# Optimization experiments

Measured on AMD Instinct MI355X. Metric: run time of the kernel, lower is better.

## Reference

```python
import jax, jax.numpy as jnp
import numpy as np

# static config (matches init_kwargs)
T_K = 3      # Time_kernel
K = 3        # spatial_kernel_side_length
C = 64       # dim_hidden
H = 4        # num_head
D = 16       # dim_head
NL = 2       # num_layers
F = 3        # dim_feature
N, S1, S2 = 32, 32, 32
P = K // 2
L1 = T_K // 2
M = T_K * K * K
EPS = 1e-5


def _neighbor_mask():
    # spatial_neighbor_mask with an all-ones city mask: offset (k1,k2) is a valid
    # neighbor of cell (s1,s2) iff it lands inside the grid.
    m = np.zeros((S1, S2, K, K), dtype=bool)
    s1 = np.arange(S1); s2 = np.arange(S2)
    for k1 in range(K):
        v1 = (s1 + k1 - P >= 0) & (s1 + k1 - P < S1)
        for k2 in range(K):
            v2 = (s2 + k2 - P >= 0) & (s2 + k2 - P < S2)
            m[:, :, k1, k2] = v1[:, None] & v2[None, :]
    mf = m.reshape(S1, S2, K * K)
    # tiled across Time_kernel, flattened in (t, k1, k2) order like the torch code
    return np.tile(mf[:, :, None, :], (1, 1, T_K, 1)).reshape(S1, S2, M)

_MASK = jnp.asarray(_neighbor_mask())


def _forward(x, W_in, b_in, W_out, b_out, Wq, bq, Wk, bk, Wv, bv):
    # BatchNorm2d (training-mode batch stats, affine = identity init)
    mean = x.mean(axis=(0, 1, 2))
    var = ((x - mean) ** 2).mean(axis=(0, 1, 2))
    h = (x - mean) * jax.lax.rsqrt(var + EPS)
    h = h @ W_in + b_in  # [N,S1,S2,C]

    for l in range(NL):
        res = h  # res_block_thickness = 1 -> residual every layer
        q = (h @ Wq[l] + bq[l]).reshape(N, S1, S2, H, D)
        # spatial unfold (nn.Unfold, padding=K//2, stride=1)
        hp = jnp.pad(h, ((0, 0), (P, P), (P, P), (0, 0)))
        u = jnp.stack([jnp.stack([hp[:, k1:k1 + S1, k2:k2 + S2, :]
                                  for k2 in range(K)]) for k1 in range(K)])  # [K,K,N,S1,S2,C]
        # time unfold (zero-padded shifts along N)
        up = jnp.pad(u, ((0, 0), (0, 0), (L1, L1), (0, 0), (0, 0), (0, 0)))
        ut = jnp.stack([up[:, :, t:t + N] for t in range(T_K)])  # [T,K,K,N,S1,S2,C]
        # per-offset single-Linear MLPs (kernel_neurons=[C,C]), batched over T,K,K
        ks = jnp.einsum('tijnabc,tijcd->nabtijd', ut, Wk[l]) + bk[l]
        vs = jnp.einsum('tijnabc,tijcd->nabtijd', ut, Wv[l]) + bv[l]
        kM = ks.reshape(N, S1, S2, M, H, D)
        vM = vs.reshape(N, S1, S2, M, H, D)
        # unscaled dot-product attention over valid neighbors (masked == dropped)
        sc = jnp.einsum('nabmhd,nabhd->nabhm', kM, q)
        sc = jnp.where(_MASK[None, :, :, None, :], sc, -1e30)
        w = jax.nn.softmax(sc, axis=-1)
        h = jnp.einsum('nabhm,nabmhd->nabhd', w, vM).reshape(N, S1, S2, C)
        h = h + res

    return h @ W_out + b_out  # [N,S1,S2,F]


def setup_inputs() -> dict:
    key = jax.random.key(0)
    k = jax.random.split(key, 11)
    s = 0.05
    return {
        'x': jax.random.normal(k[0], (N, S1, S2, F), jnp.float32),
        'W_in': jax.random.normal(k[1], (F, C), jnp.float32) * s,
        'b_in': jax.random.normal(k[2], (C,), jnp.float32) * s,
        'W_out': jax.random.normal(k[3], (C, F), jnp.float32) * s,
        'b_out': jax.random.normal(k[4], (F,), jnp.float32) * s,
        'Wq': jax.random.normal(k[5], (NL, C, C), jnp.float32) * s,
        'bq': jax.random.normal(k[6], (NL, C), jnp.float32) * s,
        'Wk': jax.random.normal(k[7], (NL, T_K, K, K, C, C), jnp.float32) * s,
        'bk': jax.random.normal(k[8], (NL, T_K, K, K, C), jnp.float32) * s,
        'Wv': jax.random.normal(k[9], (NL, T_K, K, K, C, C), jnp.float32) * s,
        'bv': jax.random.normal(k[10], (NL, T_K, K, K, C), jnp.float32) * s,
    }


def reference(x, W_in, b_in, W_out, b_out, Wq, bq, Wk, bk, Wv, bv):
    return _forward(x, W_in, b_in, W_out, b_out, Wq, bq, Wk, bk, Wv, bv)
```

## Files before the change

### kernel.cpp

```cpp
#include <hip/hip_runtime.h>
#include <hip/hip_bf16.h>


typedef short short8_t __attribute__((ext_vector_type(8)));
typedef float floatx16 __attribute__((ext_vector_type(16)));

__device__ __forceinline__ short f2bs(float f) {
    __hip_bfloat16 h = __float2bfloat16(f);
    return *reinterpret_cast<short*>(&h);
}
__device__ __forceinline__ float bs2f(short s) {
    union { unsigned u; float f; } v;
    v.u = ((unsigned)(unsigned short)s) << 16;
    return v.f;
}
__device__ __forceinline__ int hn_idx(int rowid, int chunk) {
    return rowid * 64 + ((chunk ^ (rowid & 7)) << 3);
}
__device__ __forceinline__ float half_sum(float p) {
    float a = p, b = p;
    asm("v_permlane32_swap_b32 %0, %1" : "+v"(a), "+v"(b));
    return a + b;
}

__global__ void prep_kernel(const float* __restrict__ Wq, const float* __restrict__ Wk,
                            const float* __restrict__ Wv, const float* __restrict__ bq,
                            const float* __restrict__ bk, const float* __restrict__ bv,
                            short* __restrict__ dst,
                            const float* __restrict__ x, float* __restrict__ sums) {
    if (blockIdx.x < 110) {
        __shared__ float Wf[4096];
        __shared__ float Bf[64];
        const int mat = blockIdx.x;
        const float *W, *B;
        if (mat < 2)       { W = Wq + mat * 4096;        B = bq + mat * 64; }
        else if (mat < 56) { W = Wk + (mat - 2) * 4096;  B = bk + (mat - 2) * 64; }
        else               { W = Wv + (mat - 56) * 4096; B = bv + (mat - 56) * 64; }
        const float4* W4 = (const float4*)W;
        #pragma unroll
        for (int i = 0; i < 4; ++i) {
            const int idx = threadIdx.x + i * 256;
            *(float4*)&Wf[idx * 4] = W4[idx];
        }
        if (threadIdx.x < 64) Bf[threadIdx.x] = B[threadIdx.x];
        __syncthreads();
        #pragma unroll
        for (int u = 0; u < 3; ++u) {
            const int t2 = u * 256 + threadIdx.x;
            if (t2 >= 640) break;
            const int hp = t2 / 320, rem = t2 - hp * 320;
            const int kk = rem >> 6, lane = rem & 63;
            short8_t v = {0, 0, 0, 0, 0, 0, 0, 0};
            if (kk < 4) {
                const int krow = kk * 16 + ((lane >> 5) << 3);
                const int col  = hp * 32 + (lane & 31);
                #pragma unroll
                for (int j = 0; j < 8; ++j) v[j] = f2bs(Wf[(krow + j) * 64 + col]);
            } else if ((lane >> 5) == 0) {
                const float b = Bf[hp * 32 + (lane & 31)];
                const short hi = f2bs(b);
                v[0] = hi;
                v[1] = f2bs(b - bs2f(hi));
            }
            *(short8_t*)&dst[(size_t)mat * 5120 + t2 * 8] = v;
        }
    } else {
        int bid = blockIdx.x - 110;
        int t = bid * 256 + threadIdx.x;
        const float4* x4 = (const float4*)x;
        float4 v0 = x4[t * 3 + 0], v1 = x4[t * 3 + 1], v2 = x4[t * 3 + 2];
        float vv[6];
        vv[0] = v0.x + v0.w + v1.z + v2.y;
        vv[1] = v0.y + v1.x + v1.w + v2.z;
        vv[2] = v0.z + v1.y + v2.x + v2.w;
        vv[3] = v0.x*v0.x + v0.w*v0.w + v1.z*v1.z + v2.y*v2.y;
        vv[4] = v0.y*v0.y + v1.x*v1.x + v1.w*v1.w + v2.z*v2.z;
        vv[5] = v0.z*v0.z + v1.y*v1.y + v2.x*v2.x + v2.w*v2.w;
        #pragma unroll
        for (int i = 0; i < 6; ++i) {
            #pragma unroll
            for (int off = 1; off < 64; off <<= 1) vv[i] += __shfl_xor(vv[i], off);
        }
        __shared__ float part[4][6];
        if ((threadIdx.x & 63) == 0) {
            #pragma unroll
            for (int i = 0; i < 6; ++i) part[threadIdx.x >> 6][i] = vv[i];
        }
        __syncthreads();
        if (threadIdx.x < 6)
            sums[bid * 8 + threadIdx.x] = part[0][threadIdx.x] + part[1][threadIdx.x] +
                                          part[2][threadIdx.x] + part[3][threadIdx.x];
    }
}

template <bool FIRST>
__global__ __launch_bounds__(256, 2)
void layer_fused(const float* __restrict__ x, const float* __restrict__ sums,
                 const float* __restrict__ W_in, const float* __restrict__ b_in,
                 const short* __restrict__ hbf_in, short* __restrict__ hbf_out,
                 const float* __restrict__ Wout, const float* __restrict__ bout,
                 float* __restrict__ out,
                 const short* __restrict__ wqB,
                 const short* __restrict__ wkB,
                 const short* __restrict__ wvB) {
    __shared__ short HnS[324 * 64];
    __shared__ float Waux[256];
    __shared__ float bn6[6];

    const int tid = threadIdx.x;
    const int bb0 = blockIdx.x * 4, a = blockIdx.y, nb = blockIdx.z;

    if (FIRST) {
        if (tid < 3) {
            float s = 0.f, qq = 0.f;
            #pragma unroll
            for (int p = 0; p < 32; ++p) { s += sums[p * 8 + tid]; qq += sums[p * 8 + 3 + tid]; }
            float mean = s * (1.f / 32768.f);
            float var  = qq * (1.f / 32768.f) - mean * mean;
            bn6[tid]     = mean;
            bn6[3 + tid] = rsqrtf(var + 1e-5f);
        }
        if (tid < 192) Waux[tid] = W_in[tid];
        else           Waux[tid] = b_in[tid - 192];
    } else {
        if (tid < 192)      Waux[tid] = Wout[tid];
        else if (tid < 195) Waux[tid] = bout[tid - 192];
    }
    __syncthreads();

    float mean0 = 0, mean1 = 0, mean2 = 0, rs0 = 0, rs1 = 0, rs2 = 0;
    if (FIRST) {
        mean0 = bn6[0]; mean1 = bn6[1]; mean2 = bn6[2];
        rs0 = bn6[3]; rs1 = bn6[4]; rs2 = bn6[5];
    }

    for (int id = tid; id < 2592; id += 256) {
        int rowid = id >> 3, cc = id & 7;
        int r = rowid % 18;
        int rw = rowid / 18;
        int spa = rw / 6, jcol = rw - spa * 6;
        int aa = a + spa - 1, bb = bb0 + jcol - 1;
        int n  = nb * 16 + r - 1;
        short8_t v = {0, 0, 0, 0, 0, 0, 0, 0};
        if ((unsigned)n < 32u && (unsigned)aa < 32u && (unsigned)bb < 32u) {
            int cell = (n * 32 + aa) * 32 + bb;
            if (FIRST) {
                float xn0 = (x[cell*3+0] - mean0) * rs0;
                float xn1 = (x[cell*3+1] - mean1) * rs1;
                float xn2 = (x[cell*3+2] - mean2) * rs2;
                #pragma unroll
                for (int j = 0; j < 8; ++j) {
                    int c = cc * 8 + j;
                    float h = Waux[192+c] + xn0*Waux[c] + xn1*Waux[64+c] + xn2*Waux[128+c];
                    v[j] = f2bs(h);
                }
            } else {
                v = *(const short8_t*)&hbf_in[cell * 64 + cc * 8];
            }
        }
        *(short8_t*)&HnS[hn_idx(rowid, cc)] = v;
    }
    __syncthreads();

    const int lane = tid & 63;
    const int wv4  = tid >> 6;
    const int hp   = wv4 & 1;
    const int cg   = wv4 >> 1;
    const int col  = lane & 31;
    const int e    = col & 15;
    const int ci   = col >> 4;
    const int h5   = lane >> 5;
    const int cell4 = cg * 2 + ci;
    const int bcell = bb0 + cell4;

    unsigned amask = 0;
    #pragma unroll
    for (int d = 0; d < 3; ++d) if ((unsigned)(a + d - 1) < 32u) amask |= 1u << d;
    unsigned vmask = 0;
    #pragma unroll
    for (int j = 0; j < 3; ++j) if ((unsigned)(bcell + j - 1) < 32u) vmask |= 1u << j;

    const int elane = cell4 * 18 + e;

    const short one_bf = (short)0x3F80;
    short8_t baug = {0, 0, 0, 0, 0, 0, 0, 0};
    if (h5 == 0) { baug[0] = one_bf; baug[1] = one_bf; }
    const floatx16 ZERO = {0,0,0,0, 0,0,0,0, 0,0,0,0, 0,0,0,0};

    floatx16 qv;
    {
        const int hrow = (7 + cell4) * 18 + e + 1;
        const int hb = hrow * 64, xr = hrow & 7;
        const short8_t b0 = *(const short8_t*)&HnS[hb + (((0 + h5) ^ xr) << 3)];
        const short8_t b1 = *(const short8_t*)&HnS[hb + (((2 + h5) ^ xr) << 3)];
        const short8_t b2 = *(const short8_t*)&HnS[hb + (((4 + h5) ^ xr) << 3)];
        const short8_t b3 = *(const short8_t*)&HnS[hb + (((6 + h5) ^ xr) << 3)];
        const short8_t* wqp = (const short8_t*)&wqB[hp * 2560 + lane * 8];
        qv = __builtin_amdgcn_mfma_f32_32x32x16_bf16(wqp[256], baug, ZERO, 0, 0, 0);
        qv = __builtin_amdgcn_mfma_f32_32x32x16_bf16(wqp[0],   b0, qv, 0, 0, 0);
        qv = __builtin_amdgcn_mfma_f32_32x32x16_bf16(wqp[64],  b1, qv, 0, 0, 0);
        qv = __builtin_amdgcn_mfma_f32_32x32x16_bf16(wqp[128], b2, qv, 0, 0, 0);
        qv = __builtin_amdgcn_mfma_f32_32x32x16_bf16(wqp[192], b3, qv, 0, 0, 0);
    }

    floatx16 o = {0,0,0,0, 0,0,0,0, 0,0,0,0, 0,0,0,0};
    float ssA = 0.f, ssB = 0.f;

    const short* wkBase = wkB + hp * 2560 + lane * 8;
    const short* wvBase = wvB + hp * 2560 + lane * 8;

    #pragma unroll 3
    for (int m = 0; m < 27; ++m) {
        const int t  = (m * 57) >> 9;
        const int sp = m - 9 * t;
        const int di = (sp * 11) >> 5;
        const int dj = sp - 3 * di;

        const int hrow = di * 108 + dj * 18 + t + elane;
        const int hb = hrow * 64, xr = hrow & 7;
        const short8_t b0 = *(const short8_t*)&HnS[hb + (((0 + h5) ^ xr) << 3)];
        const short8_t b1 = *(const short8_t*)&HnS[hb + (((2 + h5) ^ xr) << 3)];
        const short8_t b2 = *(const short8_t*)&HnS[hb + (((4 + h5) ^ xr) << 3)];
        const short8_t b3 = *(const short8_t*)&HnS[hb + (((6 + h5) ^ xr) << 3)];

        const short8_t wk0 = *(const short8_t*)&wkBase[m * 5120 + 0];
        const short8_t wk1 = *(const short8_t*)&wkBase[m * 5120 + 512];
        const short8_t wk2 = *(const short8_t*)&wkBase[m * 5120 + 1024];
        const short8_t wk3 = *(const short8_t*)&wkBase[m * 5120 + 1536];
        const short8_t wk4 = *(const short8_t*)&wkBase[m * 5120 + 2048];
        const short8_t wv0 = *(const short8_t*)&wvBase[m * 5120 + 0];
        const short8_t wv1 = *(const short8_t*)&wvBase[m * 5120 + 512];
        const short8_t wv2 = *(const short8_t*)&wvBase[m * 5120 + 1024];
        const short8_t wv3 = *(const short8_t*)&wvBase[m * 5120 + 1536];
        const short8_t wv4 = *(const short8_t*)&wvBase[m * 5120 + 2048];

        floatx16 kacc = __builtin_amdgcn_mfma_f32_32x32x16_bf16(wk4, baug, ZERO, 0, 0, 0);
        kacc = __builtin_amdgcn_mfma_f32_32x32x16_bf16(wk0, b0, kacc, 0, 0, 0);
        kacc = __builtin_amdgcn_mfma_f32_32x32x16_bf16(wk1, b1, kacc, 0, 0, 0);
        kacc = __builtin_amdgcn_mfma_f32_32x32x16_bf16(wk2, b2, kacc, 0, 0, 0);
        kacc = __builtin_amdgcn_mfma_f32_32x32x16_bf16(wk3, b3, kacc, 0, 0, 0);

        floatx16 vacc = __builtin_amdgcn_mfma_f32_32x32x16_bf16(wv4, baug, ZERO, 0, 0, 0);
        vacc = __builtin_amdgcn_mfma_f32_32x32x16_bf16(wv0, b0, vacc, 0, 0, 0);
        vacc = __builtin_amdgcn_mfma_f32_32x32x16_bf16(wv1, b1, vacc, 0, 0, 0);
        vacc = __builtin_amdgcn_mfma_f32_32x32x16_bf16(wv2, b2, vacc, 0, 0, 0);
        vacc = __builtin_amdgcn_mfma_f32_32x32x16_bf16(wv3, b3, vacc, 0, 0, 0);

        float pA = kacc[0] * qv[0];
        #pragma unroll
        for (int r = 1; r < 8; ++r) pA += kacc[r] * qv[r];
        float pB = kacc[8] * qv[8];
        #pragma unroll
        for (int r = 9; r < 16; ++r) pB += kacc[r] * qv[r];
        pA = half_sum(pA);
        pB = half_sum(pB);
        const float mf = (float)(((amask >> di) & (vmask >> dj)) & 1u);
        const float wA = __expf(pA) * mf;
        const float wB = __expf(pB) * mf;
        ssA += wA; ssB += wB;
        #pragma unroll
        for (int r = 0; r < 8; ++r)  o[r] += wA * vacc[r];
        #pragma unroll
        for (int r = 8; r < 16; ++r) o[r] += wB * vacc[r];
    }

    {
        const float invA = 1.0f / ssA;
        const float invB = 1.0f / ssB;
        #pragma unroll
        for (int r = 0; r < 8; ++r)  o[r] *= invA;
        #pragma unroll
        for (int r = 8; r < 16; ++r) o[r] *= invB;
    }

    const int n = nb * 16 + e;
    const int cell = (n * 32 + a) * 32 + bcell;
    if (FIRST) {
        const float xn0 = (x[cell*3+0] - mean0) * rs0;
        const float xn1 = (x[cell*3+1] - mean1) * rs1;
        const float xn2 = (x[cell*3+2] - mean2) * rs2;
        #pragma unroll
        for (int g = 0; g < 4; ++g) {
            short4 hb4; short* hbp = (short*)&hb4;
            #pragma unroll
            for (int i = 0; i < 4; ++i) {
                const int c = hp * 32 + g * 8 + 4 * h5 + i;
                const float res = Waux[192+c] + xn0*Waux[c] + xn1*Waux[64+c] + xn2*Waux[128+c];
                hbp[i] = f2bs(o[g * 4 + i] + res);
            }
            *(short4*)&hbf_out[cell * 64 + hp * 32 + g * 8 + 4 * h5] = hb4;
        }
    } else {
        __syncthreads();
        float* hf = (float*)HnS;
        const int bcol = cell4 * 16 + e;
        #pragma unroll
        for (int g = 0; g < 4; ++g) {
            const short4 hb4 = *(const short4*)&hbf_in[cell * 64 + hp * 32 + g * 8 + 4 * h5];
            float4 tv = make_float4(o[g*4+0] + bs2f(hb4.x), o[g*4+1] + bs2f(hb4.y),
                                    o[g*4+2] + bs2f(hb4.z), o[g*4+3] + bs2f(hb4.w));
            *(float4*)&hf[bcol * 68 + hp * 32 + g * 8 + 4 * h5] = tv;
        }
        __syncthreads();
        if (tid < 192) {
            const int rowglob = tid / 3, f = tid - rowglob * 3;
            float acc = Waux[192 + f];
            #pragma unroll 8
            for (int cc = 0; cc < 64; ++cc) acc += hf[rowglob * 68 + cc] * Waux[cc * 3 + f];
            const int cellb = bb0 + (rowglob >> 4), row = rowglob & 15;
            out[(((nb * 16 + row) * 32 + a) * 32 + cellb) * 3 + f] = acc;
        }
    }
}

extern "C" void kernel_launch(void* const* d_in, const int* in_sizes, int n_in,
                              void* d_out, int out_size, void* d_ws, size_t ws_size,
                              hipStream_t stream) {
    const float* x     = (const float*)d_in[0];
    const float* W_in  = (const float*)d_in[1];
    const float* b_in  = (const float*)d_in[2];
    const float* W_out = (const float*)d_in[3];
    const float* b_out = (const float*)d_in[4];
    const float* Wq    = (const float*)d_in[5];
    const float* bq    = (const float*)d_in[6];
    const float* Wk    = (const float*)d_in[7];
    const float* bk    = (const float*)d_in[8];
    const float* Wv    = (const float*)d_in[9];
    const float* bv    = (const float*)d_in[10];

    float* ws    = (float*)d_ws;
    float* sums  = ws;
    short* h1bf  = (short*)(ws + 256);
    short* wB    = h1bf + 2097152;
    float* out   = (float*)d_out;

    prep_kernel<<<142, 256, 0, stream>>>(Wq, Wk, Wv, bq, bk, bv, wB, x, sums);

    const short* wq0 = wB;                const short* wq1 = wB + 5120;
    const short* wk0 = wB + 2 * 5120;     const short* wk1 = wB + (2 + 27) * 5120;
    const short* wv0 = wB + 56 * 5120;    const short* wv1 = wB + (56 + 27) * 5120;

    dim3 grid(8, 32, 2);
    layer_fused<true><<<grid, 256, 0, stream>>>(
        x, sums, W_in, b_in, nullptr, h1bf, nullptr, nullptr, nullptr,
        wq0, wk0, wv0);
    layer_fused<false><<<grid, 256, 0, stream>>>(
        nullptr, nullptr, nullptr, nullptr, h1bf, nullptr, W_out, b_out, out,
        wq1, wk1, wv1);
}
```

Measured before the change: 133.2 us.

## Cover all 32 time steps per block so each weight fragment feeds two tiles

Each block now covers the full temporal range (32 rows plus halo) instead of splitting it across two z-blocks, so every loaded K/V weight fragment is reused for two 16-row time tiles. This halves global weight traffic per output and drops the duplicated halo rows. In exchange the grid shrinks to 256 blocks, the shared tile nearly doubles, per-thread register use grows with two accumulator sets, and launch bounds drop to one block per SM. That may reduce occupancy and latency hiding. The dot-product reduction is also reassociated into a shallower tree.

After: 164.6 us. +23.6%, slower.

```diff
diff --git a/kernel.cpp b/kernel.cpp
--- a/kernel.cpp
+++ b/kernel.cpp
@@ -94,7 +94,7 @@
 }
 
 template <bool FIRST>
-__global__ __launch_bounds__(256, 2)
+__global__ __launch_bounds__(256, 1)
 void layer_fused(const float* __restrict__ x, const float* __restrict__ sums,
                  const float* __restrict__ W_in, const float* __restrict__ b_in,
                  const short* __restrict__ hbf_in, short* __restrict__ hbf_out,
@@ -103,12 +103,12 @@
                  const short* __restrict__ wqB,
                  const short* __restrict__ wkB,
                  const short* __restrict__ wvB) {
-    __shared__ short HnS[324 * 64];
+    __shared__ short HnS[612 * 64];
     __shared__ float Waux[256];
     __shared__ float bn6[6];
 
     const int tid = threadIdx.x;
-    const int bb0 = blockIdx.x * 4, a = blockIdx.y, nb = blockIdx.z;
+    const int bb0 = blockIdx.x * 4, a = blockIdx.y;
 
     if (FIRST) {
         if (tid < 3) {
@@ -134,13 +134,12 @@
         rs0 = bn6[3]; rs1 = bn6[4]; rs2 = bn6[5];
     }
 
-    for (int id = tid; id < 2592; id += 256) {
+    for (int id = tid; id < 4896; id += 256) {
         int rowid = id >> 3, cc = id & 7;
-        int r = rowid % 18;
-        int rw = rowid / 18;
+        int rw = rowid / 34, r = rowid - rw * 34;
         int spa = rw / 6, jcol = rw - spa * 6;
         int aa = a + spa - 1, bb = bb0 + jcol - 1;
-        int n  = nb * 16 + r - 1;
+        int n  = r - 1;
         short8_t v = {0, 0, 0, 0, 0, 0, 0, 0};
         if ((unsigned)n < 32u && (unsigned)aa < 32u && (unsigned)bb < 32u) {
             int cell = (n * 32 + aa) * 32 + bb;
@@ -165,12 +164,11 @@
     const int lane = tid & 63;
     const int wv4  = tid >> 6;
     const int hp   = wv4 & 1;
-    const int cg   = wv4 >> 1;
-    const int col  = lane & 31;
-    const int e    = col & 15;
-    const int ci   = col >> 4;
+    const int cp   = wv4 >> 1;
+    const int e    = lane & 15;
+    const int ci   = (lane >> 4) & 1;
     const int h5   = lane >> 5;
-    const int cell4 = cg * 2 + ci;
+    const int cell4 = cp * 2 + ci;
     const int bcell = bb0 + cell4;
 
     unsigned amask = 0;
@@ -180,135 +178,167 @@
     #pragma unroll
     for (int j = 0; j < 3; ++j) if ((unsigned)(bcell + j - 1) < 32u) vmask |= 1u << j;
 
-    const int elane = cell4 * 18 + e;
+    const int eb = cell4 * 34 + e;
 
     const short one_bf = (short)0x3F80;
     short8_t baug = {0, 0, 0, 0, 0, 0, 0, 0};
     if (h5 == 0) { baug[0] = one_bf; baug[1] = one_bf; }
     const floatx16 ZERO = {0,0,0,0, 0,0,0,0, 0,0,0,0, 0,0,0,0};
 
-    floatx16 qv;
+    floatx16 qv0, qv1;
     {
-        const int hrow = (7 + cell4) * 18 + e + 1;
-        const int hb = hrow * 64, xr = hrow & 7;
-        const short8_t b0 = *(const short8_t*)&HnS[hb + (((0 + h5) ^ xr) << 3)];
-        const short8_t b1 = *(const short8_t*)&HnS[hb + (((2 + h5) ^ xr) << 3)];
-        const short8_t b2 = *(const short8_t*)&HnS[hb + (((4 + h5) ^ xr) << 3)];
-        const short8_t b3 = *(const short8_t*)&HnS[hb + (((6 + h5) ^ xr) << 3)];
         const short8_t* wqp = (const short8_t*)&wqB[hp * 2560 + lane * 8];
-        qv = __builtin_amdgcn_mfma_f32_32x32x16_bf16(wqp[256], baug, ZERO, 0, 0, 0);
-        qv = __builtin_amdgcn_mfma_f32_32x32x16_bf16(wqp[0],   b0, qv, 0, 0, 0);
-        qv = __builtin_amdgcn_mfma_f32_32x32x16_bf16(wqp[64],  b1, qv, 0, 0, 0);
-        qv = __builtin_amdgcn_mfma_f32_32x32x16_bf16(wqp[128], b2, qv, 0, 0, 0);
-        qv = __builtin_amdgcn_mfma_f32_32x32x16_bf16(wqp[192], b3, qv, 0, 0, 0);
-    }
-
-    floatx16 o = {0,0,0,0, 0,0,0,0, 0,0,0,0, 0,0,0,0};
-    float ssA = 0.f, ssB = 0.f;
+#define Q_SET(QV, TS)                                                              \
+        {                                                                          \
+            const int hrow = 7 * 34 + eb + (TS) * 16 + 1;                          \
+            const int hb = hrow * 64, xr = hrow & 7;                               \
+            const short8_t b0 = *(const short8_t*)&HnS[hb + (((0 + h5) ^ xr) << 3)];\
+            const short8_t b1 = *(const short8_t*)&HnS[hb + (((2 + h5) ^ xr) << 3)];\
+            const short8_t b2 = *(const short8_t*)&HnS[hb + (((4 + h5) ^ xr) << 3)];\
+            const short8_t b3 = *(const short8_t*)&HnS[hb + (((6 + h5) ^ xr) << 3)];\
+            QV = __builtin_amdgcn_mfma_f32_32x32x16_bf16(wqp[256], baug, ZERO, 0, 0, 0);\
+            QV = __builtin_amdgcn_mfma_f32_32x32x16_bf16(wqp[0],   b0, QV, 0, 0, 0);\
+            QV = __builtin_amdgcn_mfma_f32_32x32x16_bf16(wqp[64],  b1, QV, 0, 0, 0);\
+            QV = __builtin_amdgcn_mfma_f32_32x32x16_bf16(wqp[128], b2, QV, 0, 0, 0);\
+            QV = __builtin_amdgcn_mfma_f32_32x32x16_bf16(wqp[192], b3, QV, 0, 0, 0);\
+        }
+        Q_SET(qv0, 0)
+        Q_SET(qv1, 1)
+#undef Q_SET
+    }
+
+    floatx16 o0 = {0,0,0,0, 0,0,0,0, 0,0,0,0, 0,0,0,0};
+    floatx16 o1 = {0,0,0,0, 0,0,0,0, 0,0,0,0, 0,0,0,0};
+    float ssA0 = 0.f, ssB0 = 0.f, ssA1 = 0.f, ssB1 = 0.f;
 
     const short* wkBase = wkB + hp * 2560 + lane * 8;
     const short* wvBase = wvB + hp * 2560 + lane * 8;
 
-    #pragma unroll 3
-    for (int m = 0; m < 27; ++m) {
-        const int t  = (m * 57) >> 9;
-        const int sp = m - 9 * t;
-        const int di = (sp * 11) >> 5;
-        const int dj = sp - 3 * di;
-
-        const int hrow = di * 108 + dj * 18 + t + elane;
-        const int hb = hrow * 64, xr = hrow & 7;
-        const short8_t b0 = *(const short8_t*)&HnS[hb + (((0 + h5) ^ xr) << 3)];
-        const short8_t b1 = *(const short8_t*)&HnS[hb + (((2 + h5) ^ xr) << 3)];
-        const short8_t b2 = *(const short8_t*)&HnS[hb + (((4 + h5) ^ xr) << 3)];
-        const short8_t b3 = *(const short8_t*)&HnS[hb + (((6 + h5) ^ xr) << 3)];
-
-        const short8_t wk0 = *(const short8_t*)&wkBase[m * 5120 + 0];
-        const short8_t wk1 = *(const short8_t*)&wkBase[m * 5120 + 512];
-        const short8_t wk2 = *(const short8_t*)&wkBase[m * 5120 + 1024];
-        const short8_t wk3 = *(const short8_t*)&wkBase[m * 5120 + 1536];
-        const short8_t wk4 = *(const short8_t*)&wkBase[m * 5120 + 2048];
-        const short8_t wv0 = *(const short8_t*)&wvBase[m * 5120 + 0];
-        const short8_t wv1 = *(const short8_t*)&wvBase[m * 5120 + 512];
-        const short8_t wv2 = *(const short8_t*)&wvBase[m * 5120 + 1024];
-        const short8_t wv3 = *(const short8_t*)&wvBase[m * 5120 + 1536];
-        const short8_t wv4 = *(const short8_t*)&wvBase[m * 5120 + 2048];
-
-        floatx16 kacc = __builtin_amdgcn_mfma_f32_32x32x16_bf16(wk4, baug, ZERO, 0, 0, 0);
-        kacc = __builtin_amdgcn_mfma_f32_32x32x16_bf16(wk0, b0, kacc, 0, 0, 0);
-        kacc = __builtin_amdgcn_mfma_f32_32x32x16_bf16(wk1, b1, kacc, 0, 0, 0);
-        kacc = __builtin_amdgcn_mfma_f32_32x32x16_bf16(wk2, b2, kacc, 0, 0, 0);
-        kacc = __builtin_amdgcn_mfma_f32_32x32x16_bf16(wk3, b3, kacc, 0, 0, 0);
-
-        floatx16 vacc = __builtin_amdgcn_mfma_f32_32x32x16_bf16(wv4, baug, ZERO, 0, 0, 0);
-        vacc = __builtin_amdgcn_mfma_f32_32x32x16_bf16(wv0, b0, vacc, 0, 0, 0);
-        vacc = __builtin_amdgcn_mfma_f32_32x32x16_bf16(wv1, b1, vacc, 0, 0, 0);
-        vacc = __builtin_amdgcn_mfma_f32_32x32x16_bf16(wv2, b2, vacc, 0, 0, 0);
-        vacc = __builtin_amdgcn_mfma_f32_32x32x16_bf16(wv3, b3, vacc, 0, 0, 0);
-
-        float pA = kacc[0] * qv[0];
-        #pragma unroll
-        for (int r = 1; r < 8; ++r) pA += kacc[r] * qv[r];
-        float pB = kacc[8] * qv[8];
-        #pragma unroll
-        for (int r = 9; r < 16; ++r) pB += kacc[r] * qv[r];
-        pA = half_sum(pA);
-        pB = half_sum(pB);
-        const float mf = (float)(((amask >> di) & (vmask >> dj)) & 1u);
-        const float wA = __expf(pA) * mf;
-        const float wB = __expf(pB) * mf;
-        ssA += wA; ssB += wB;
-        #pragma unroll
-        for (int r = 0; r < 8; ++r)  o[r] += wA * vacc[r];
-        #pragma unroll
-        for (int r = 8; r < 16; ++r) o[r] += wB * vacc[r];
-    }
+#define KV_SET(HROWB, QV, O, SSA, SSB)                                             \
+    {                                                                              \
+        const int hrow_ = (HROWB);                                                 \
+        const int hb_ = hrow_ * 64, xr_ = hrow_ & 7;                               \
+        const short8_t b0_ = *(const short8_t*)&HnS[hb_ + (((0 + h5) ^ xr_) << 3)];\
+        const short8_t b1_ = *(const short8_t*)&HnS[hb_ + (((2 + h5) ^ xr_) << 3)];\
+        const short8_t b2_ = *(const short8_t*)&HnS[hb_ + (((4 + h5) ^ xr_) << 3)];\
+        const short8_t b3_ = *(const short8_t*)&HnS[hb_ + (((6 + h5) ^ xr_) << 3)];\
+        floatx16 kacc_ = __builtin_amdgcn_mfma_f32_32x32x16_bf16(wk4, baug, ZERO, 0, 0, 0);\
+        kacc_ = __builtin_amdgcn_mfma_f32_32x32x16_bf16(wk0, b0_, kacc_, 0, 0, 0); \
+        kacc_ = __builtin_amdgcn_mfma_f32_32x32x16_bf16(wk1, b1_, kacc_, 0, 0, 0); \
+        kacc_ = __builtin_amdgcn_mfma_f32_32x32x16_bf16(wk2, b2_, kacc_, 0, 0, 0); \
+        kacc_ = __builtin_amdgcn_mfma_f32_32x32x16_bf16(wk3, b3_, kacc_, 0, 0, 0); \
+        floatx16 vacc_ = __builtin_amdgcn_mfma_f32_32x32x16_bf16(wv4, baug, ZERO, 0, 0, 0);\
+        vacc_ = __builtin_amdgcn_mfma_f32_32x32x16_bf16(wv0, b0_, vacc_, 0, 0, 0); \
+        vacc_ = __builtin_amdgcn_mfma_f32_32x32x16_bf16(wv1, b1_, vacc_, 0, 0, 0); \
+        vacc_ = __builtin_amdgcn_mfma_f32_32x32x16_bf16(wv2, b2_, vacc_, 0, 0, 0); \
+        vacc_ = __builtin_amdgcn_mfma_f32_32x32x16_bf16(wv3, b3_, vacc_, 0, 0, 0); \
+        float pA0_ = kacc_[0] * QV[0] + kacc_[1] * QV[1];                          \
+        float pA1_ = kacc_[2] * QV[2] + kacc_[3] * QV[3];                          \
+        float pA2_ = kacc_[4] * QV[4] + kacc_[5] * QV[5];                          \
+        float pA3_ = kacc_[6] * QV[6] + kacc_[7] * QV[7];                          \
+        float pB0_ = kacc_[8] * QV[8] + kacc_[9] * QV[9];                          \
+        float pB1_ = kacc_[10] * QV[10] + kacc_[11] * QV[11];                      \
+        float pB2_ = kacc_[12] * QV[12] + kacc_[13] * QV[13];                      \
+        float pB3_ = kacc_[14] * QV[14] + kacc_[15] * QV[15];                      \
+        float pA_ = (pA0_ + pA1_) + (pA2_ + pA3_);                                 \
+        float pB_ = (pB0_ + pB1_) + (pB2_ + pB3_);                                 \
+        pA_ = half_sum(pA_);                                                       \
+        pB_ = half_sum(pB_);                                                       \
+        const float wA_ = __expf(pA_) * mf;                                        \
+        const float wB_ = __expf(pB_) * mf;                                        \
+        SSA += wA_; SSB += wB_;                                                    \
+        _Pragma("unroll")                                                          \
+        for (int r = 0; r < 8; ++r)  O[r] += wA_ * vacc_[r];                       \
+        _Pragma("unroll")                                                          \
+        for (int r = 8; r < 16; ++r) O[r] += wB_ * vacc_[r];                       \
+    }
+
+    for (int t = 0; t < 3; ++t) {
+        const short* wkT = wkBase + t * 46080;
+        const short* wvT = wvBase + t * 46080;
+        #pragma unroll
+        for (int sp = 0; sp < 9; ++sp) {
+            const int di = sp / 3, dj = sp - 3 * (sp / 3);
+            const short8_t wk0 = *(const short8_t*)&wkT[sp * 5120 + 0];
+            const short8_t wk1 = *(const short8_t*)&wkT[sp * 5120 + 512];
+            const short8_t wk2 = *(const short8_t*)&wkT[sp * 5120 + 1024];
+            const short8_t wk3 = *(const short8_t*)&wkT[sp * 5120 + 1536];
+            const short8_t wk4 = *(const short8_t*)&wkT[sp * 5120 + 2048];
+            const short8_t wv0 = *(const short8_t*)&wvT[sp * 5120 + 0];
+            const short8_t wv1 = *(const short8_t*)&wvT[sp * 5120 + 512];
+            const short8_t wv2 = *(const short8_t*)&wvT[sp * 5120 + 1024];
+            const short8_t wv3 = *(const short8_t*)&wvT[sp * 5120 + 1536];
+            const short8_t wv4 = *(const short8_t*)&wvT[sp * 5120 + 2048];
+            const float mf = (float)(((amask >> di) & (vmask >> dj)) & 1u);
+            const int hrowb = (di * 6 + dj) * 34 + t + eb;
+            KV_SET(hrowb,      qv0, o0, ssA0, ssB0)
+            KV_SET(hrowb + 16, qv1, o1, ssA1, ssB1)
+        }
+    }
+#undef KV_SET
 
     {
-        const float invA = 1.0f / ssA;
-        const float invB = 1.0f / ssB;
-        #pragma unroll
-        for (int r = 0; r < 8; ++r)  o[r] *= invA;
-        #pragma unroll
-        for (int r = 8; r < 16; ++r) o[r] *= invB;
-    }
-
-    const int n = nb * 16 + e;
-    const int cell = (n * 32 + a) * 32 + bcell;
+        const float iA0 = 1.0f / ssA0, iB0 = 1.0f / ssB0;
+        const float iA1 = 1.0f / ssA1, iB1 = 1.0f / ssB1;
+        #pragma unroll
+        for (int r = 0; r < 8; ++r)  { o0[r] *= iA0; o1[r] *= iA1; }
+        #pragma unroll
+        for (int r = 8; r < 16; ++r) { o0[r] *= iB0; o1[r] *= iB1; }
+    }
+
     if (FIRST) {
-        const float xn0 = (x[cell*3+0] - mean0) * rs0;
-        const float xn1 = (x[cell*3+1] - mean1) * rs1;
-        const float xn2 = (x[cell*3+2] - mean2) * rs2;
-        #pragma unroll
-        for (int g = 0; g < 4; ++g) {
-            short4 hb4; short* hbp = (short*)&hb4;
-            #pragma unroll
-            for (int i = 0; i < 4; ++i) {
-                const int c = hp * 32 + g * 8 + 4 * h5 + i;
-                const float res = Waux[192+c] + xn0*Waux[c] + xn1*Waux[64+c] + xn2*Waux[128+c];
-                hbp[i] = f2bs(o[g * 4 + i] + res);
-            }
-            *(short4*)&hbf_out[cell * 64 + hp * 32 + g * 8 + 4 * h5] = hb4;
-        }
+#define EPI_FIRST(OV, TS)                                                          \
+        {                                                                          \
+            const int n_ = (TS) * 16 + e;                                          \
+            const int cell_ = (n_ * 32 + a) * 32 + bcell;                          \
+            const float xn0_ = (x[cell_*3+0] - mean0) * rs0;                       \
+            const float xn1_ = (x[cell_*3+1] - mean1) * rs1;                       \
+            const float xn2_ = (x[cell_*3+2] - mean2) * rs2;                       \
+            _Pragma("unroll")                                                      \
+            for (int g = 0; g < 4; ++g) {                                          \
+                short4 hb4_; short* hbp_ = (short*)&hb4_;                          \
+                _Pragma("unroll")                                                  \
+                for (int i = 0; i < 4; ++i) {                                      \
+                    const int c_ = hp * 32 + g * 8 + 4 * h5 + i;                   \
+                    const float res_ = Waux[192+c_] + xn0_*Waux[c_] +              \
+                                       xn1_*Waux[64+c_] + xn2_*Waux[128+c_];       \
+                    hbp_[i] = f2bs(OV[g * 4 + i] + res_);                          \
+                }                                                                  \
+                *(short4*)&hbf_out[cell_ * 64 + hp * 32 + g * 8 + 4 * h5] = hb4_;  \
+            }                                                                      \
+        }
+        EPI_FIRST(o0, 0)
+        EPI_FIRST(o1, 1)
+#undef EPI_FIRST
     } else {
         __syncthreads();
         float* hf = (float*)HnS;
-        const int bcol = cell4 * 16 + e;
-        #pragma unroll
-        for (int g = 0; g < 4; ++g) {
-            const short4 hb4 = *(const short4*)&hbf_in[cell * 64 + hp * 32 + g * 8 + 4 * h5];
-            float4 tv = make_float4(o[g*4+0] + bs2f(hb4.x), o[g*4+1] + bs2f(hb4.y),
-                                    o[g*4+2] + bs2f(hb4.z), o[g*4+3] + bs2f(hb4.w));
-            *(float4*)&hf[bcol * 68 + hp * 32 + g * 8 + 4 * h5] = tv;
-        }
+#define EPI_SECOND(OV, TS)                                                         \
+        {                                                                          \
+            const int n_ = (TS) * 16 + e;                                          \
+            const int cell_ = (n_ * 32 + a) * 32 + bcell;                          \
+            const int bcol_ = cell4 * 32 + n_;                                     \
+            _Pragma("unroll")                                                      \
+            for (int g = 0; g < 4; ++g) {                                          \
+                const short4 hb4_ = *(const short4*)&hbf_in[cell_ * 64 + hp * 32 + g * 8 + 4 * h5];\
+                float4 tv_ = make_float4(OV[g*4+0] + bs2f(hb4_.x),                 \
+                                         OV[g*4+1] + bs2f(hb4_.y),                 \
+                                         OV[g*4+2] + bs2f(hb4_.z),                 \
+                                         OV[g*4+3] + bs2f(hb4_.w));                \
+                *(float4*)&hf[bcol_ * 68 + hp * 32 + g * 8 + 4 * h5] = tv_;        \
+            }                                                                      \
+        }
+        EPI_SECOND(o0, 0)
+        EPI_SECOND(o1, 1)
+#undef EPI_SECOND
         __syncthreads();
-        if (tid < 192) {
-            const int rowglob = tid / 3, f = tid - rowglob * 3;
+        for (int oid = tid; oid < 384; oid += 256) {
+            const int rowglob = oid / 3, f = oid - rowglob * 3;
             float acc = Waux[192 + f];
             #pragma unroll 8
             for (int cc = 0; cc < 64; ++cc) acc += hf[rowglob * 68 + cc] * Waux[cc * 3 + f];
-            const int cellb = bb0 + (rowglob >> 4), row = rowglob & 15;
-            out[(((nb * 16 + row) * 32 + a) * 32 + cellb) * 3 + f] = acc;
+            const int cellb = bb0 + (rowglob >> 5), n = rowglob & 31;
+            out[((n * 32 + a) * 32 + cellb) * 3 + f] = acc;
         }
     }
 }
@@ -340,7 +370,7 @@
     const short* wk0 = wB + 2 * 5120;     const short* wk1 = wB + (2 + 27) * 5120;
     const short* wv0 = wB + 56 * 5120;    const short* wv1 = wB + (56 + 27) * 5120;
 
-    dim3 grid(8, 32, 2);
+    dim3 grid(8, 32);
     layer_fused<true><<<grid, 256, 0, stream>>>(
         x, sums, W_in, b_in, nullptr, h1bf, nullptr, nullptr, nullptr,
         wq0, wk0, wv0);
```

## Fuse both layer kernels into one persistent launch with a grid barrier

Applied to the files above, without the earlier changes.

Merges the two per-layer kernel launches into a single 512-block kernel. An atomic-counter grid barrier separates layer 1 from layer 2, and the counter is cleared with a memset before the launch. The aim is to remove one kernel launch and its drain/fill gap. In exchange, all 512 blocks must be co-resident for the spin barrier to avoid deadlock (256 CUs × 2 blocks on MI355X), and it adds spin-wait and fence overhead.

After: 251.8 us. 89.0% more time.

```diff
diff --git a/kernel.cpp b/kernel.cpp
--- a/kernel.cpp
+++ b/kernel.cpp
@@ -94,21 +94,17 @@
 }
 
 template <bool FIRST>
-__global__ __launch_bounds__(256, 2)
-void layer_fused(const float* __restrict__ x, const float* __restrict__ sums,
-                 const float* __restrict__ W_in, const float* __restrict__ b_in,
-                 const short* __restrict__ hbf_in, short* __restrict__ hbf_out,
-                 const float* __restrict__ Wout, const float* __restrict__ bout,
-                 float* __restrict__ out,
-                 const short* __restrict__ wqB,
-                 const short* __restrict__ wkB,
-                 const short* __restrict__ wvB) {
-    __shared__ short HnS[324 * 64];
-    __shared__ float Waux[256];
-    __shared__ float bn6[6];
-
-    const int tid = threadIdx.x;
-    const int bb0 = blockIdx.x * 4, a = blockIdx.y, nb = blockIdx.z;
+__device__ __forceinline__ void layer_phase(
+        int blk, int tid,
+        const float* __restrict__ x, const float* __restrict__ sums,
+        const float* __restrict__ W_in, const float* __restrict__ b_in,
+        const short* __restrict__ hbf_in, short* __restrict__ hbf_out,
+        const float* __restrict__ Wout, const float* __restrict__ bout,
+        float* __restrict__ out,
+        const short* __restrict__ wqB, const short* __restrict__ wkB,
+        const short* __restrict__ wvB,
+        short* HnS, float* Waux, float* bn6) {
+    const int bb0 = (blk & 7) * 4, a = (blk >> 3) & 31, nb = blk >> 8;
 
     if (FIRST) {
         if (tid < 3) {
@@ -165,12 +161,11 @@
     const int lane = tid & 63;
     const int wv4  = tid >> 6;
     const int hp   = wv4 & 1;
-    const int cg   = wv4 >> 1;
-    const int col  = lane & 31;
-    const int e    = col & 15;
-    const int ci   = col >> 4;
+    const int cgp  = wv4 >> 1;
+    const int e    = lane & 15;
+    const int ci   = (lane >> 4) & 1;
     const int h5   = lane >> 5;
-    const int cell4 = cg * 2 + ci;
+    const int cell4 = cgp * 2 + ci;
     const int bcell = bb0 + cell4;
 
     unsigned amask = 0;
@@ -313,6 +308,43 @@
     }
 }
 
+__device__ __forceinline__ void grid_bar(unsigned* cnt, unsigned target) {
+    __threadfence();
+    __syncthreads();
+    if (threadIdx.x == 0) {
+        atomicAdd(cnt, 1u);
+        while (atomicAdd(cnt, 0u) < target) __builtin_amdgcn_s_sleep(8);
+    }
+    __syncthreads();
+    __threadfence();
+}
+
+__global__ __launch_bounds__(256, 2)
+void fused_l1l2(const float* __restrict__ x, const float* __restrict__ sums,
+                const float* __restrict__ W_in, const float* __restrict__ b_in,
+                const float* __restrict__ Wout, const float* __restrict__ bout,
+                float* __restrict__ out, short* __restrict__ h1bf,
+                const short* __restrict__ wB, unsigned* __restrict__ cnt) {
+    __shared__ short HnS[324 * 64];
+    __shared__ float Waux[256];
+    __shared__ float bn6[6];
+
+    const int tid = threadIdx.x;
+    const int blk = blockIdx.x;
+
+    const short* wq0 = wB;                const short* wq1 = wB + 5120;
+    const short* wk0 = wB + 2 * 5120;     const short* wk1 = wB + (2 + 27) * 5120;
+    const short* wv0 = wB + 56 * 5120;    const short* wv1 = wB + (56 + 27) * 5120;
+
+    layer_phase<true>(blk, tid, x, sums, W_in, b_in, nullptr, h1bf,
+                      nullptr, nullptr, nullptr, wq0, wk0, wv0, HnS, Waux, bn6);
+
+    grid_bar(cnt, 512u);
+
+    layer_phase<false>(blk, tid, nullptr, nullptr, nullptr, nullptr, h1bf, nullptr,
+                       Wout, bout, out, wq1, wk1, wv1, HnS, Waux, bn6);
+}
+
 extern "C" void kernel_launch(void* const* d_in, const int* in_sizes, int n_in,
                               void* d_out, int out_size, void* d_ws, size_t ws_size,
                               hipStream_t stream) {
@@ -332,19 +364,11 @@
     float* sums  = ws;
     short* h1bf  = (short*)(ws + 256);
     short* wB    = h1bf + 2097152;
+    unsigned* cnt = (unsigned*)(wB + 110 * 5120);
     float* out   = (float*)d_out;
 
+    hipMemsetAsync(cnt, 0, 4, stream);
     prep_kernel<<<142, 256, 0, stream>>>(Wq, Wk, Wv, bq, bk, bv, wB, x, sums);
-
-    const short* wq0 = wB;                const short* wq1 = wB + 5120;
-    const short* wk0 = wB + 2 * 5120;     const short* wk1 = wB + (2 + 27) * 5120;
-    const short* wv0 = wB + 56 * 5120;    const short* wv1 = wB + (56 + 27) * 5120;
-
-    dim3 grid(8, 32, 2);
-    layer_fused<true><<<grid, 256, 0, stream>>>(
-        x, sums, W_in, b_in, nullptr, h1bf, nullptr, nullptr, nullptr,
-        wq0, wk0, wv0);
-    layer_fused<false><<<grid, 256, 0, stream>>>(
-        nullptr, nullptr, nullptr, nullptr, h1bf, nullptr, W_out, b_out, out,
-        wq1, wk1, wv1);
-}
+    fused_l1l2<<<512, 256, 0, stream>>>(x, sums, W_in, b_in, W_out, b_out,
+                                        out, h1bf, wB, cnt);
+}
```
